# Kernel tuning notes

Measured on AMD Instinct MI355X. Metric: run time of the kernel, lower is better.

## Reference

```python
import jax, jax.numpy as jnp
import numpy as np

N = 100000
E = 1600000
NUM_GRAPHS = 64
EPS = 1e-5


def setup_inputs() -> dict:
    key = jax.random.key(0)
    ks = jax.random.split(key, 8)
    x = jax.random.normal(ks[0], (N, 128), dtype=jnp.float32)
    edge_index = jax.random.randint(ks[1], (2, E), 0, N, dtype=jnp.int64)
    batch = jnp.sort(jax.random.randint(ks[2], (N,), 0, NUM_GRAPHS, dtype=jnp.int64))
    W1 = jax.random.normal(ks[3], (128, 128), dtype=jnp.float32) * (1.0 / np.sqrt(128))
    W2 = jax.random.normal(ks[4], (128, 128), dtype=jnp.float32) * (1.0 / np.sqrt(128))
    W3 = jax.random.normal(ks[5], (128, 32), dtype=jnp.float32) * (1.0 / np.sqrt(128))
    return {
        'x': x, 'edge_index': edge_index, 'batch': batch,
        'W1': W1, 'b1': jnp.zeros((128,), jnp.float32),
        'W2': W2, 'b2': jnp.zeros((128,), jnp.float32),
        'W3': W3, 'b3': jnp.zeros((32,), jnp.float32),
        'gamma1': jnp.ones((128,), jnp.float32), 'beta1': jnp.zeros((128,), jnp.float32),
        'gamma2': jnp.ones((128,), jnp.float32), 'beta2': jnp.zeros((128,), jnp.float32),
    }


def _gcn_norm(edge_index, n_nodes):
    # PyG GCNConv default: add self-loops, symmetric normalization.
    loop = jnp.arange(n_nodes, dtype=edge_index.dtype)
    src = jnp.concatenate([edge_index[0], loop])  # [E+N]
    dst = jnp.concatenate([edge_index[1], loop])
    deg = jax.ops.segment_sum(jnp.ones_like(dst, dtype=jnp.float32), dst,
                              num_segments=n_nodes)
    dinv = jnp.where(deg > 0, jax.lax.rsqrt(deg), 0.0)
    norm = dinv[src] * dinv[dst]  # [E+N]
    return src, dst, norm


def _gcn_conv(x, W, b, src, dst, norm, n_nodes):
    h = x @ W                                   # [N, d_out] dense GEMM
    msg = h[src] * norm[:, None]                # gather + scale  [E+N, d_out]
    out = jax.ops.segment_sum(msg, dst, num_segments=n_nodes)  # scatter-add
    return out + b


def _batchnorm(x, gamma, beta):
    # Training-mode BatchNorm1d: batch stats over node dim, biased variance.
    mean = jnp.mean(x, axis=0)
    var = jnp.var(x, axis=0)
    return (x - mean) * jax.lax.rsqrt(var + EPS) * gamma + beta


def reference(x, edge_index, batch, W1, b1, W2, b2, W3, b3,
              gamma1, beta1, gamma2, beta2):
    src, dst, norm = _gcn_norm(edge_index, N)
    h = _gcn_conv(x, W1, b1, src, dst, norm, N)
    h = jax.nn.relu(_batchnorm(h, gamma1, beta1))  # dropout is identity (eval)
    h = _gcn_conv(h, W2, b2, src, dst, norm, N)
    h = jax.nn.relu(_batchnorm(h, gamma2, beta2))
    h = _gcn_conv(h, W3, b3, src, dst, norm, N)
    # global_mean_pool over graph ids
    sums = jax.ops.segment_sum(h, batch, num_segments=NUM_GRAPHS)  # [G, out]
    cnts = jax.ops.segment_sum(jnp.ones((N,), jnp.float32), batch,
                               num_segments=NUM_GRAPHS)
    pooled = sums / jnp.maximum(cnts, 1.0)[:, None]
    return jax.nn.sigmoid(pooled)
```

## Files before the change

### kernel.cpp

```cpp
#include <hip/hip_runtime.h>
#include <math.h>

#define NGRAPH 64
#define EPS_BN 1e-5f
#define BN_BLOCKS 512

typedef unsigned int uint32;
typedef unsigned short ushort16;
typedef __attribute__((ext_vector_type(8))) short short8v;
typedef __attribute__((ext_vector_type(4))) float float4v;

__device__ __forceinline__ float bf2f(uint32 u16) {
    return __uint_as_float(u16 << 16);
}
__device__ __forceinline__ ushort16 f2bf(float f) {
    uint32 u = __float_as_uint(f);
    return (ushort16)((u + 0x7fffu + ((u >> 16) & 1u)) >> 16);
}
__device__ __forceinline__ uint32 pack2(float lo, float hi) {
    return (uint32)f2bf(lo) | ((uint32)f2bf(hi) << 16);
}

#define SC_EPB 8
__global__ __launch_bounds__(256) void k_cnt_w(const int* __restrict__ dst, int* __restrict__ cnt,
                                               int ne, int wsz) {
    const int w = blockIdx.x & 7;
    const int chunk = blockIdx.x >> 3;
    const int wlo = w * wsz;
    const int whi = wlo + wsz;
    int base = chunk * (256 * SC_EPB) + threadIdx.x;
    #pragma unroll
    for (int j = 0; j < SC_EPB; ++j) {
        int i = base + j * 256;
        if (i < ne) {
            int d = dst[i];
            if (d >= wlo && d < whi) atomicAdd(&cnt[d], 1);
        }
    }
}

__global__ __launch_bounds__(1024) void k_scan1(const int* __restrict__ cnt,
                                                int* __restrict__ rowstart,
                                                int* __restrict__ blocksum,
                                                float* __restrict__ dinv, int n) {
    __shared__ int sh[1024];
    const int tid = threadIdx.x;
    const int i = blockIdx.x * 1024 + tid;
    int v = (i < n) ? cnt[i] : 0;
    if (i < n) dinv[i] = rsqrtf((float)(v + 1));
    sh[tid] = v;
    __syncthreads();
    for (int off = 1; off < 1024; off <<= 1) {
        int t = (tid >= off) ? sh[tid - off] : 0;
        __syncthreads();
        sh[tid] += t;
        __syncthreads();
    }
    if (i < n) rowstart[i] = sh[tid] - v;
    if (tid == 1023) blocksum[blockIdx.x] = sh[1023];
}

__global__ __launch_bounds__(1024) void k_scan2(int* __restrict__ blocksum, int nb) {
    __shared__ int sh[1024];
    const int tid = threadIdx.x;
    int v = (tid < nb) ? blocksum[tid] : 0;
    sh[tid] = v;
    __syncthreads();
    for (int off = 1; off < 1024; off <<= 1) {
        int t = (tid >= off) ? sh[tid - off] : 0;
        __syncthreads();
        sh[tid] += t;
        __syncthreads();
    }
    if (tid < nb) blocksum[tid] = sh[tid] - v;
}

__global__ __launch_bounds__(256) void k_scan3(int* __restrict__ rowstart,
                                               int* __restrict__ rowcur,
                                               const int* __restrict__ blocksum, int n) {
    int i = blockIdx.x * 256 + threadIdx.x;
    if (i < n) {
        int v = rowstart[i] + blocksum[i >> 10];
        rowstart[i] = v;
        rowcur[i] = v;
    }
}

__global__ __launch_bounds__(256) void k_scatter_w(const int* __restrict__ src,
                                                   const int* __restrict__ dst,
                                                   int* __restrict__ rowcur,
                                                   int* __restrict__ esrc,
                                                   int ne, int wsz) {
    const int w = blockIdx.x & 7;
    const int chunk = blockIdx.x >> 3;
    const int wlo = w * wsz;
    const int whi = wlo + wsz;
    int base = chunk * (256 * SC_EPB) + threadIdx.x;
    #pragma unroll
    for (int j = 0; j < SC_EPB; ++j) {
        int i = base + j * 256;
        if (i < ne) {
            int d = dst[i];
            if (d >= wlo && d < whi) {
                int pos = atomicAdd(&rowcur[d], 1);
                esrc[pos] = src[i];
            }
        }
    }
}

__global__ __launch_bounds__(256) void k_wprep_all(const float* __restrict__ W1,
                                                   const float* __restrict__ W2,
                                                   const float* __restrict__ W3,
                                                   ushort16* __restrict__ wt1,
                                                   ushort16* __restrict__ wt2,
                                                   ushort16* __restrict__ wt3) {
    int i = blockIdx.x * 256 + threadIdx.x;
    if (i < 16384) {
        int c = i >> 7, k = i & 127;
        wt1[i] = f2bf(W1[k * 128 + c]);
    } else if (i < 32768) {
        int j = i - 16384;
        int c = j >> 7, k = j & 127;
        wt2[j] = f2bf(W2[k * 128 + c]);
    } else if (i < 36864) {
        int j = i - 32768;
        int c = j >> 7, k = j & 127;
        wt3[j] = f2bf(W3[k * 32 + c]);
    }
}

template<int COLS, bool BN, bool AF32>
__global__ __launch_bounds__(256) void k_gemm_mfma(const void* __restrict__ Av,
                                                   const ushort16* __restrict__ Wt,
                                                   const float* __restrict__ ss,
                                                   ushort16* __restrict__ C, int nrows) {
    constexpr int K = 128;
    constexpr int LDK = K + 8;
    __shared__ ushort16 As[64 * LDK];
    __shared__ ushort16 Bs[COLS * LDK];
    const int tid = threadIdx.x;

    {
        const uint4* wg = (const uint4*)Wt;
        for (int i = tid; i < COLS * (K / 8); i += 256) {
            int r = i >> 4, c8 = i & 15;
            *(uint4*)&Bs[r * LDK + c8 * 8] = wg[i];
        }
    }

    const int w = tid >> 6;
    const int l = tid & 63;
    const int lr = l & 15;
    const int lg = l >> 4;
    constexpr int CT = COLS / 16;

    #pragma unroll
    for (int half = 0; half < 2; ++half) {
        const int row0 = blockIdx.x * 128 + half * 64;
        if (half) __syncthreads();
        if constexpr (AF32) {
            const float* A = (const float*)Av;
            for (int i = tid; i < 64 * (K / 4); i += 256) {
                int r = i >> 5, c4 = i & 31;
                float4 a;
                if (row0 + r < nrows) a = *(const float4*)&A[(size_t)(row0 + r) * K + c4 * 4];
                else a = make_float4(0.f, 0.f, 0.f, 0.f);
                if (BN) {
                    float4 sc = *(const float4*)&ss[c4 * 4];
                    float4 sh = *(const float4*)&ss[128 + c4 * 4];
                    a.x = fmaxf(fmaf(a.x, sc.x, sh.x), 0.f);
                    a.y = fmaxf(fmaf(a.y, sc.y, sh.y), 0.f);
                    a.z = fmaxf(fmaf(a.z, sc.z, sh.z), 0.f);
                    a.w = fmaxf(fmaf(a.w, sc.w, sh.w), 0.f);
                }
                ushort4 o;
                o.x = f2bf(a.x); o.y = f2bf(a.y); o.z = f2bf(a.z); o.w = f2bf(a.w);
                *(ushort4*)&As[r * LDK + c4 * 4] = o;
            }
        } else {
            const uint4* Ag = (const uint4*)Av;
            for (int i = tid; i < 64 * (K / 8); i += 256) {
                int r = i >> 4, c8 = i & 15;
                uint4 u;
                if (row0 + r < nrows) u = Ag[(size_t)(row0 + r) * 16 + c8];
                else u = make_uint4(0, 0, 0, 0);
                if (BN) {
                    uint32 wv[4] = {u.x, u.y, u.z, u.w};
                    #pragma unroll
                    for (int t = 0; t < 4; ++t) {
                        int f = c8 * 8 + t * 2;
                        float lo = fmaxf(fmaf(bf2f(wv[t] & 0xffffu), ss[f],     ss[128 + f]),     0.f);
                        float hi = fmaxf(fmaf(bf2f(wv[t] >> 16),     ss[f + 1], ss[128 + f + 1]), 0.f);
                        wv[t] = pack2(lo, hi);
                    }
                    u.x = wv[0]; u.y = wv[1]; u.z = wv[2]; u.w = wv[3];
                }
                *(uint4*)&As[r * LDK + c8 * 8] = u;
            }
        }
        __syncthreads();

        float4v acc[CT] = {};
        short8v afrag[4];
        #pragma unroll
        for (int kk = 0; kk < 4; ++kk)
            afrag[kk] = *(const short8v*)&As[(w * 16 + lr) * LDK + kk * 32 + lg * 8];
        #pragma unroll
        for (int kk = 0; kk < 4; ++kk) {
            #pragma unroll
            for (int ct = 0; ct < CT; ++ct) {
                short8v b = *(const short8v*)&Bs[(ct * 16 + lr) * LDK + kk * 32 + lg * 8];
                acc[ct] = __builtin_amdgcn_mfma_f32_16x16x32_bf16(afrag[kk], b, acc[ct], 0, 0, 0);
            }
        }
        #pragma unroll
        for (int ct = 0; ct < CT; ++ct) {
            #pragma unroll
            for (int r = 0; r < 4; ++r) {
                int gr = row0 + w * 16 + lg * 4 + r;
                if (gr < nrows) C[(size_t)gr * COLS + ct * 16 + lr] = f2bf(acc[ct][r]);
            }
        }
    }
}

template<int COLS>
__global__ __launch_bounds__(256) void k_agg_csr(const ushort16* __restrict__ h,
                                                 const int* __restrict__ rowstart,
                                                 const int* __restrict__ cnt,
                                                 const int* __restrict__ esrc,
                                                 const float* __restrict__ dinv,
                                                 uint32* __restrict__ out, int n) {
    constexpr int TPN = COLS / 2;
    const uint32* __restrict__ hu = (const uint32*)h;
    int gt = blockIdx.x * 256 + threadIdx.x;
    int node = gt / TPN;
    if (node >= n) return;
    int lane = gt % TPN;

    float di = dinv[node];
    uint32 p = hu[(size_t)node * TPN + lane];
    float ax = bf2f(p & 0xffffu) * di * di;
    float ay = bf2f(p >> 16) * di * di;

    const int beg = rowstart[node];
    const int end = beg + cnt[node];
    int e = beg;
    for (; e + 8 <= end; e += 8) {
        int s[8]; uint32 pp[8]; float w[8];
        #pragma unroll
        for (int j = 0; j < 8; ++j) s[j] = esrc[e + j];
        #pragma unroll
        for (int j = 0; j < 8; ++j) pp[j] = hu[(size_t)s[j] * TPN + lane];
        #pragma unroll
        for (int j = 0; j < 8; ++j) w[j] = dinv[s[j]] * di;
        #pragma unroll
        for (int j = 0; j < 8; ++j) {
            ax = fmaf(bf2f(pp[j] & 0xffffu), w[j], ax);
            ay = fmaf(bf2f(pp[j] >> 16), w[j], ay);
        }
    }
    for (; e < end; ++e) {
        int s0 = esrc[e];
        float w0 = dinv[s0] * di;
        uint32 p0 = hu[(size_t)s0 * TPN + lane];
        ax = fmaf(bf2f(p0 & 0xffffu), w0, ax);
        ay = fmaf(bf2f(p0 >> 16), w0, ay);
    }
    out[(size_t)node * TPN + lane] = pack2(ax, ay);
}

__global__ __launch_bounds__(256) void k_bn_stats1(const uint32* __restrict__ x,
                                                   float* __restrict__ partials, int n) {
    const int cp = threadIdx.x & 63;
    const int rl = threadIdx.x >> 6;
    float s0 = 0.f, s1 = 0.f, q0 = 0.f, q1 = 0.f;
    for (int r = blockIdx.x * 4 + rl; r < n; r += BN_BLOCKS * 4) {
        uint32 u = x[(size_t)r * 64 + cp];
        float lo = bf2f(u & 0xffffu), hi = bf2f(u >> 16);
        s0 += lo; s1 += hi;
        q0 = fmaf(lo, lo, q0); q1 = fmaf(hi, hi, q1);
    }
    __shared__ float shs[4 * 128];
    __shared__ float shq[4 * 128];
    shs[rl * 128 + 2 * cp] = s0; shs[rl * 128 + 2 * cp + 1] = s1;
    shq[rl * 128 + 2 * cp] = q0; shq[rl * 128 + 2 * cp + 1] = q1;
    __syncthreads();
    int f = threadIdx.x;
    if (f < 128) {
        float s = shs[f] + shs[128 + f] + shs[256 + f] + shs[384 + f];
        float q = shq[f] + shq[128 + f] + shq[256 + f] + shq[384 + f];
        partials[(size_t)blockIdx.x * 256 + f] = s;
        partials[(size_t)blockIdx.x * 256 + 128 + f] = q;
    }
}

__global__ __launch_bounds__(256) void k_bn_stats2(const float* __restrict__ partials,
                                                   float* __restrict__ stats) {
    int j = threadIdx.x;
    float acc = 0.f;
    int r0 = blockIdx.x * (BN_BLOCKS / 8);
    for (int r = 0; r < BN_BLOCKS / 8; ++r)
        acc += partials[(size_t)(r0 + r) * 256 + j];
    atomicAdd(&stats[j], acc);
}

__global__ __launch_bounds__(128) void k_bn_final(const float* __restrict__ stats,
                                                  const float* __restrict__ gamma,
                                                  const float* __restrict__ beta,
                                                  float* __restrict__ ss, int n) {
    int f = threadIdx.x;
    float inv_n = 1.0f / (float)n;
    float mean = stats[f] * inv_n;
    float var = stats[128 + f] * inv_n - mean * mean;
    float scale = gamma[f] * rsqrtf(var + EPS_BN);
    ss[f] = scale;
    ss[128 + f] = beta[f] - mean * scale;
}

#define POOL_SLICE 128
__global__ __launch_bounds__(256) void k_pool2(const uint32* __restrict__ h3,
                                               const int* __restrict__ batch,
                                               float* __restrict__ sums,
                                               float* __restrict__ cnt, int n) {
    const int fp = threadIdx.x & 15;
    const int sub = threadIdx.x >> 4;
    int node0 = blockIdx.x * (16 * POOL_SLICE) + sub * POOL_SLICE;
    if (node0 >= n) return;
    int node1 = min(node0 + POOL_SLICE, n);

    int cur_g = batch[node0];
    float a0 = 0.f, a1 = 0.f, c = 0.f;
    for (int i = node0; i < node1; ++i) {
        int g = batch[i];
        if (g != cur_g) {
            atomicAdd(&sums[cur_g * 32 + 2 * fp], a0);
            atomicAdd(&sums[cur_g * 32 + 2 * fp + 1], a1);
            if (fp == 0) atomicAdd(&cnt[cur_g], c);
            a0 = 0.f; a1 = 0.f; c = 0.f; cur_g = g;
        }
        uint32 u = h3[(size_t)i * 16 + fp];
        a0 += bf2f(u & 0xffffu);
        a1 += bf2f(u >> 16);
        c += 1.f;
    }
    atomicAdd(&sums[cur_g * 32 + 2 * fp], a0);
    atomicAdd(&sums[cur_g * 32 + 2 * fp + 1], a1);
    if (fp == 0) atomicAdd(&cnt[cur_g], c);
}

__global__ __launch_bounds__(256) void k_final(const float* __restrict__ sums,
                                               const float* __restrict__ cnt,
                                               const float* __restrict__ b3,
                                               float* __restrict__ out) {
    int i = blockIdx.x * 256 + threadIdx.x;
    if (i >= NGRAPH * 32) return;
    int g = i >> 5;
    int f = i & 31;
    float c = fmaxf(cnt[g], 1.0f);
    float v = sums[i] / c + b3[f];
    out[i] = 1.0f / (1.0f + expf(-v));
}

extern "C" void kernel_launch(void* const* d_in, const int* in_sizes, int n_in,
                              void* d_out, int out_size, void* d_ws, size_t ws_size,
                              hipStream_t stream) {
    const float* x      = (const float*)d_in[0];
    const int*   eidx   = (const int*)d_in[1];
    const int*   batch  = (const int*)d_in[2];
    const float* W1     = (const float*)d_in[3];
    const float* W2     = (const float*)d_in[5];
    const float* W3     = (const float*)d_in[7];
    const float* b3     = (const float*)d_in[8];
    const float* gamma1 = (const float*)d_in[9];
    const float* beta1  = (const float*)d_in[10];
    const float* gamma2 = (const float*)d_in[11];
    const float* beta2  = (const float*)d_in[12];

    const int N = in_sizes[0] / 128;
    const int E = in_sizes[1] / 2;
    const int* src = eidx;
    const int* dst = eidx + E;

    size_t off = 0;
    auto carve = [&](size_t bytes) {
        char* p = (char*)d_ws + off;
        off += (bytes + 511) & ~(size_t)511;
        return p;
    };
    const size_t NB = (size_t)N * 128 * sizeof(float);
    ushort16* bufA  = (ushort16*)carve(NB / 2);
    uint32* bufB    = (uint32*)carve(NB / 2);
    int*   cnt      = (int*)carve((size_t)N * 4);
    int*   rowstart = (int*)carve((size_t)N * 4);
    int*   rowcur   = (int*)carve((size_t)N * 4);
    float* dinv     = (float*)carve((size_t)N * 4);
    int*   esrc     = (int*)carve((size_t)E * 4);
    ushort16* wt1   = (ushort16*)carve(128 * 128 * 2);
    ushort16* wt2   = (ushort16*)carve(128 * 128 * 2);
    ushort16* wt3   = (ushort16*)carve(32 * 128 * 2);
    float* stats    = (float*)carve(256 * 4);
    float* ss1      = (float*)carve(256 * 4);
    float* ss2      = (float*)carve(256 * 4);
    float* partials = (float*)carve((size_t)BN_BLOCKS * 256 * 4);
    int*   blocksum = (int*)carve(1024 * 4);
    float* psum     = (float*)carve(NGRAPH * 32 * 4);
    float* pcnt     = (float*)carve(NGRAPH * 4);
    (void)ws_size; (void)n_in; (void)out_size;

    const int nblkN   = (N + 255) / 256;
    const int nbScan  = (N + 1023) / 1024;
    const int nbGemm  = (N + 127) / 128;
    const int nblkAgg128 = ((size_t)N * 64 + 255) / 256;
    const int nblkAgg32  = ((size_t)N * 16 + 255) / 256;
    const int nblkPool   = (N + 16 * POOL_SLICE - 1) / (16 * POOL_SLICE);
    const int wsz        = (N + 7) / 8;
    const int nbScat     = ((E + 256 * SC_EPB - 1) / (256 * SC_EPB)) * 8;

    k_wprep_all<<<(36864 + 255) / 256, 256, 0, stream>>>(W1, W2, W3, wt1, wt2, wt3);

    hipMemsetAsync(cnt, 0, (size_t)N * 4, stream);
    k_cnt_w<<<nbScat, 256, 0, stream>>>(dst, cnt, E, wsz);
    k_scan1<<<nbScan, 1024, 0, stream>>>(cnt, rowstart, blocksum, dinv, N);
    k_scan2<<<1, 1024, 0, stream>>>(blocksum, nbScan);
    k_scan3<<<nblkN, 256, 0, stream>>>(rowstart, rowcur, blocksum, N);
    k_scatter_w<<<nbScat, 256, 0, stream>>>(src, dst, rowcur, esrc, E, wsz);

    k_gemm_mfma<128, false, true><<<nbGemm, 256, 0, stream>>>(x, wt1, nullptr, bufA, N);
    k_agg_csr<128><<<nblkAgg128, 256, 0, stream>>>(bufA, rowstart, cnt, esrc, dinv, bufB, N);
    k_bn_stats1<<<BN_BLOCKS, 256, 0, stream>>>(bufB, partials, N);
    hipMemsetAsync(stats, 0, 256 * 4, stream);
    k_bn_stats2<<<8, 256, 0, stream>>>(partials, stats);
    k_bn_final<<<1, 128, 0, stream>>>(stats, gamma1, beta1, ss1, N);

    k_gemm_mfma<128, true, false><<<nbGemm, 256, 0, stream>>>(bufB, wt2, ss1, bufA, N);
    k_agg_csr<128><<<nblkAgg128, 256, 0, stream>>>(bufA, rowstart, cnt, esrc, dinv, bufB, N);
    k_bn_stats1<<<BN_BLOCKS, 256, 0, stream>>>(bufB, partials, N);
    hipMemsetAsync(stats, 0, 256 * 4, stream);
    k_bn_stats2<<<8, 256, 0, stream>>>(partials, stats);
    k_bn_final<<<1, 128, 0, stream>>>(stats, gamma2, beta2, ss2, N);

    k_gemm_mfma<32, true, false><<<nbGemm, 256, 0, stream>>>(bufB, wt3, ss2, bufA, N);
    k_agg_csr<32><<<nblkAgg32, 256, 0, stream>>>(bufA, rowstart, cnt, esrc, dinv, bufB, N);

    hipMemsetAsync(psum, 0, NGRAPH * 32 * 4, stream);
    hipMemsetAsync(pcnt, 0, NGRAPH * 4, stream);
    k_pool2<<<nblkPool, 256, 0, stream>>>(bufB, batch, psum, pcnt, N);
    k_final<<<(NGRAPH * 32 + 255) / 256, 256, 0, stream>>>(psum, pcnt, b3, (float*)d_out);
}
```

Baseline: 481.8 us.

## Pre-scale GEMM rows by dinv, simplify aggregation, fold memsets and BN finalize

Multiplies each GEMM output row by the source node's dinv, so the aggregation kernel becomes a plain sum followed by one multiply by the destination dinv. This removes the per-edge dinv gather and multiply. The aggregation loop also drops from 8-way to 4-way unrolling and uses readfirstlane for the row bounds. Separately, the memsets are folded into existing kernels (cnt zeroed in wprep, psum/pcnt zeroed in scan2), and BN stats reduction and finalize merge into one kernel without atomics. Together these cut launch count, at the cost of slightly different bf16 rounding from pre-scaling and possibly less memory-level parallelism in the gather loop.

```diff
diff --git a/kernel.cpp b/kernel.cpp
--- a/kernel.cpp
+++ b/kernel.cpp
@@ -60,7 +60,9 @@
     if (tid == 1023) blocksum[blockIdx.x] = sh[1023];
 }
 
-__global__ __launch_bounds__(1024) void k_scan2(int* __restrict__ blocksum, int nb) {
+__global__ __launch_bounds__(1024) void k_scan2(int* __restrict__ blocksum, int nb,
+                                                float* __restrict__ psum,
+                                                float* __restrict__ pcnt) {
     __shared__ int sh[1024];
     const int tid = threadIdx.x;
     int v = (tid < nb) ? blocksum[tid] : 0;
@@ -73,6 +75,8 @@
         __syncthreads();
     }
     if (tid < nb) blocksum[tid] = sh[tid] - v;
+    for (int i = tid; i < NGRAPH * 32; i += 1024) psum[i] = 0.f;
+    if (tid < NGRAPH) pcnt[tid] = 0.f;
 }
 
 __global__ __launch_bounds__(256) void k_scan3(int* __restrict__ rowstart,
@@ -114,7 +118,8 @@
                                                    const float* __restrict__ W3,
                                                    ushort16* __restrict__ wt1,
                                                    ushort16* __restrict__ wt2,
-                                                   ushort16* __restrict__ wt3) {
+                                                   ushort16* __restrict__ wt3,
+                                                   int* __restrict__ cnt, int n) {
     int i = blockIdx.x * 256 + threadIdx.x;
     if (i < 16384) {
         int c = i >> 7, k = i & 127;
@@ -128,12 +133,14 @@
         int c = j >> 7, k = j & 127;
         wt3[j] = f2bf(W3[k * 32 + c]);
     }
+    if (i < n) cnt[i] = 0;
 }
 
 template<int COLS, bool BN, bool AF32>
 __global__ __launch_bounds__(256) void k_gemm_mfma(const void* __restrict__ Av,
                                                    const ushort16* __restrict__ Wt,
                                                    const float* __restrict__ ss,
+                                                   const float* __restrict__ dinv,
                                                    ushort16* __restrict__ C, int nrows) {
     constexpr int K = 128;
     constexpr int LDK = K + 8;
@@ -215,11 +222,13 @@
             }
         }
         #pragma unroll
-        for (int ct = 0; ct < CT; ++ct) {
-            #pragma unroll
-            for (int r = 0; r < 4; ++r) {
-                int gr = row0 + w * 16 + lg * 4 + r;
-                if (gr < nrows) C[(size_t)gr * COLS + ct * 16 + lr] = f2bf(acc[ct][r]);
+        for (int r = 0; r < 4; ++r) {
+            int gr = row0 + w * 16 + lg * 4 + r;
+            if (gr < nrows) {
+                float dv = dinv[gr];
+                #pragma unroll
+                for (int ct = 0; ct < CT; ++ct)
+                    C[(size_t)gr * COLS + ct * 16 + lr] = f2bf(acc[ct][r] * dv);
             }
         }
     }
@@ -241,34 +250,35 @@
 
     float di = dinv[node];
     uint32 p = hu[(size_t)node * TPN + lane];
-    float ax = bf2f(p & 0xffffu) * di * di;
-    float ay = bf2f(p >> 16) * di * di;
-
-    const int beg = rowstart[node];
-    const int end = beg + cnt[node];
+    float ax = bf2f(p & 0xffffu);
+    float ay = bf2f(p >> 16);
+
+    int beg = rowstart[node];
+    int dg = cnt[node];
+    if constexpr (TPN == 64) {
+        beg = __builtin_amdgcn_readfirstlane(beg);
+        dg = __builtin_amdgcn_readfirstlane(dg);
+    }
+    const int end = beg + dg;
     int e = beg;
-    for (; e + 8 <= end; e += 8) {
-        int s[8]; uint32 pp[8]; float w[8];
-        #pragma unroll
-        for (int j = 0; j < 8; ++j) s[j] = esrc[e + j];
-        #pragma unroll
-        for (int j = 0; j < 8; ++j) pp[j] = hu[(size_t)s[j] * TPN + lane];
-        #pragma unroll
-        for (int j = 0; j < 8; ++j) w[j] = dinv[s[j]] * di;
-        #pragma unroll
-        for (int j = 0; j < 8; ++j) {
-            ax = fmaf(bf2f(pp[j] & 0xffffu), w[j], ax);
-            ay = fmaf(bf2f(pp[j] >> 16), w[j], ay);
-        }
+    for (; e + 4 <= end; e += 4) {
+        int s0 = esrc[e], s1 = esrc[e + 1], s2 = esrc[e + 2], s3 = esrc[e + 3];
+        uint32 p0 = hu[(size_t)s0 * TPN + lane];
+        uint32 p1 = hu[(size_t)s1 * TPN + lane];
+        uint32 p2 = hu[(size_t)s2 * TPN + lane];
+        uint32 p3 = hu[(size_t)s3 * TPN + lane];
+        ax += bf2f(p0 & 0xffffu); ay += bf2f(p0 >> 16);
+        ax += bf2f(p1 & 0xffffu); ay += bf2f(p1 >> 16);
+        ax += bf2f(p2 & 0xffffu); ay += bf2f(p2 >> 16);
+        ax += bf2f(p3 & 0xffffu); ay += bf2f(p3 >> 16);
     }
     for (; e < end; ++e) {
         int s0 = esrc[e];
-        float w0 = dinv[s0] * di;
         uint32 p0 = hu[(size_t)s0 * TPN + lane];
-        ax = fmaf(bf2f(p0 & 0xffffu), w0, ax);
-        ay = fmaf(bf2f(p0 >> 16), w0, ay);
-    }
-    out[(size_t)node * TPN + lane] = pack2(ax, ay);
+        ax += bf2f(p0 & 0xffffu);
+        ay += bf2f(p0 >> 16);
+    }
+    out[(size_t)node * TPN + lane] = pack2(ax * di, ay * di);
 }
 
 __global__ __launch_bounds__(256) void k_bn_stats1(const uint32* __restrict__ x,
@@ -297,26 +307,32 @@
 }
 
 __global__ __launch_bounds__(256) void k_bn_stats2(const float* __restrict__ partials,
-                                                   float* __restrict__ stats) {
-    int j = threadIdx.x;
-    float acc = 0.f;
-    int r0 = blockIdx.x * (BN_BLOCKS / 8);
-    for (int r = 0; r < BN_BLOCKS / 8; ++r)
-        acc += partials[(size_t)(r0 + r) * 256 + j];
-    atomicAdd(&stats[j], acc);
-}
-
-__global__ __launch_bounds__(128) void k_bn_final(const float* __restrict__ stats,
-                                                  const float* __restrict__ gamma,
-                                                  const float* __restrict__ beta,
-                                                  float* __restrict__ ss, int n) {
-    int f = threadIdx.x;
-    float inv_n = 1.0f / (float)n;
-    float mean = stats[f] * inv_n;
-    float var = stats[128 + f] * inv_n - mean * mean;
-    float scale = gamma[f] * rsqrtf(var + EPS_BN);
-    ss[f] = scale;
-    ss[128 + f] = beta[f] - mean * scale;
+                                                   const float* __restrict__ gamma,
+                                                   const float* __restrict__ beta,
+                                                   float* __restrict__ ss, int n) {
+    const int f16 = threadIdx.x & 15;
+    const int rl = threadIdx.x >> 4;
+    const int f = blockIdx.x * 16 + f16;
+    float s = 0.f, q = 0.f;
+    for (int r = rl; r < BN_BLOCKS; r += 16) {
+        s += partials[(size_t)r * 256 + f];
+        q += partials[(size_t)r * 256 + 128 + f];
+    }
+    __shared__ float shs[256], shq[256];
+    shs[threadIdx.x] = s;
+    shq[threadIdx.x] = q;
+    __syncthreads();
+    if (rl == 0) {
+        float S = 0.f, Q = 0.f;
+        #pragma unroll
+        for (int r = 0; r < 16; ++r) { S += shs[r * 16 + f16]; Q += shq[r * 16 + f16]; }
+        float inv_n = 1.0f / (float)n;
+        float mean = S * inv_n;
+        float var = Q * inv_n - mean * mean;
+        float scale = gamma[f] * rsqrtf(var + EPS_BN);
+        ss[f] = scale;
+        ss[128 + f] = beta[f] - mean * scale;
+    }
 }
 
 #define POOL_SLICE 128
@@ -400,7 +416,6 @@
     ushort16* wt1   = (ushort16*)carve(128 * 128 * 2);
     ushort16* wt2   = (ushort16*)carve(128 * 128 * 2);
     ushort16* wt3   = (ushort16*)carve(32 * 128 * 2);
-    float* stats    = (float*)carve(256 * 4);
     float* ss1      = (float*)carve(256 * 4);
     float* ss2      = (float*)carve(256 * 4);
     float* partials = (float*)carve((size_t)BN_BLOCKS * 256 * 4);
@@ -417,35 +432,29 @@
     const int nblkPool   = (N + 16 * POOL_SLICE - 1) / (16 * POOL_SLICE);
     const int wsz        = (N + 7) / 8;
     const int nbScat     = ((E + 256 * SC_EPB - 1) / (256 * SC_EPB)) * 8;
-
-    k_wprep_all<<<(36864 + 255) / 256, 256, 0, stream>>>(W1, W2, W3, wt1, wt2, wt3);
-
-    hipMemsetAsync(cnt, 0, (size_t)N * 4, stream);
+    const int nbWprep    = (((36864 > N) ? 36864 : N) + 255) / 256;
+
+    k_wprep_all<<<nbWprep, 256, 0, stream>>>(W1, W2, W3, wt1, wt2, wt3, cnt, N);
+
     k_cnt_w<<<nbScat, 256, 0, stream>>>(dst, cnt, E, wsz);
     k_scan1<<<nbScan, 1024, 0, stream>>>(cnt, rowstart, blocksum, dinv, N);
-    k_scan2<<<1, 1024, 0, stream>>>(blocksum, nbScan);
+    k_scan2<<<1, 1024, 0, stream>>>(blocksum, nbScan, psum, pcnt);
     k_scan3<<<nblkN, 256, 0, stream>>>(rowstart, rowcur, blocksum, N);
     k_scatter_w<<<nbScat, 256, 0, stream>>>(src, dst, rowcur, esrc, E, wsz);
 
-    k_gemm_mfma<128, false, true><<<nbGemm, 256, 0, stream>>>(x, wt1, nullptr, bufA, N);
+    k_gemm_mfma<128, false, true><<<nbGemm, 256, 0, stream>>>(x, wt1, nullptr, dinv, bufA, N);
     k_agg_csr<128><<<nblkAgg128, 256, 0, stream>>>(bufA, rowstart, cnt, esrc, dinv, bufB, N);
     k_bn_stats1<<<BN_BLOCKS, 256, 0, stream>>>(bufB, partials, N);
-    hipMemsetAsync(stats, 0, 256 * 4, stream);
-    k_bn_stats2<<<8, 256, 0, stream>>>(partials, stats);
-    k_bn_final<<<1, 128, 0, stream>>>(stats, gamma1, beta1, ss1, N);
-
-    k_gemm_mfma<128, true, false><<<nbGemm, 256, 0, stream>>>(bufB, wt2, ss1, bufA, N);
+    k_bn_stats2<<<8, 256, 0, stream>>>(partials, gamma1, beta1, ss1, N);
+
+    k_gemm_mfma<128, true, false><<<nbGemm, 256, 0, stream>>>(bufB, wt2, ss1, dinv, bufA, N);
     k_agg_csr<128><<<nblkAgg128, 256, 0, stream>>>(bufA, rowstart, cnt, esrc, dinv, bufB, N);
     k_bn_stats1<<<BN_BLOCKS, 256, 0, stream>>>(bufB, partials, N);
-    hipMemsetAsync(stats, 0, 256 * 4, stream);
-    k_bn_stats2<<<8, 256, 0, stream>>>(partials, stats);
-    k_bn_final<<<1, 128, 0, stream>>>(stats, gamma2, beta2, ss2, N);
-
-    k_gemm_mfma<32, true, false><<<nbGemm, 256, 0, stream>>>(bufB, wt3, ss2, bufA, N);
+    k_bn_stats2<<<8, 256, 0, stream>>>(partials, gamma2, beta2, ss2, N);
+
+    k_gemm_mfma<32, true, false><<<nbGemm, 256, 0, stream>>>(bufB, wt3, ss2, dinv, bufA, N);
     k_agg_csr<32><<<nblkAgg32, 256, 0, stream>>>(bufA, rowstart, cnt, esrc, dinv, bufB, N);
 
-    hipMemsetAsync(psum, 0, NGRAPH * 32 * 4, stream);
-    hipMemsetAsync(pcnt, 0, NGRAPH * 4, stream);
     k_pool2<<<nblkPool, 256, 0, stream>>>(bufB, batch, psum, pcnt, N);
     k_final<<<(NGRAPH * 32 + 255) / 256, 256, 0, stream>>>(psum, pcnt, b3, (float*)d_out);
 }
```

Result: faster. 459.9 us (-4.5%).
